# Optimization experiments

Measured on AMD Instinct MI355X. Metric: run time of the kernel, lower is better.

## Reference

```python
import jax, jax.numpy as jnp
import numpy as np

N = 1_000_000          # query points
L = 6                  # positional encoding terms
ND = 3                 # n_dims
C = 16                 # n_features
G = 96                 # feature grid resolution per axis
NODES = 128            # decoder width
IN_DIM = C + L * ND * 2  # 52
VOL_MIN, VOL_MAX = 0.0, 1.0


def setup_inputs() -> dict:
    key = jax.random.key(0)
    ks = jax.random.split(key, 8)
    x = jax.random.uniform(ks[0], (N, ND), jnp.float32, minval=-1.0, maxval=1.0)
    feature_grid = jax.random.uniform(ks[1], (C, G, G, G), jnp.float32)  # torch.rand init
    s = 0.05
    w_in = jax.random.normal(ks[2], (IN_DIM, NODES), jnp.float32) * s
    w_h0 = jax.random.normal(ks[3], (NODES, NODES), jnp.float32) * s
    w_h1 = jax.random.normal(ks[4], (NODES, NODES), jnp.float32) * s
    w_h2 = jax.random.normal(ks[5], (NODES, NODES), jnp.float32) * s
    w_out = jax.random.normal(ks[6], (NODES, 1), jnp.float32) * s
    return {"x": x, "feature_grid": feature_grid, "w_in": w_in,
            "w_h0": w_h0, "w_h1": w_h1, "w_h2": w_h2, "w_out": w_out}


def _trilinear(grid, pts):
    """grid_sample 3D, bilinear, align_corners=True. grid [C,D,H,W], pts [N,3]
    with channel order (x->W, y->H, z->D) as in torch. Returns [N, C]."""
    Cc, D, H, W = grid.shape
    fx = (pts[:, 0] + 1.0) * 0.5 * (W - 1)
    fy = (pts[:, 1] + 1.0) * 0.5 * (H - 1)
    fz = (pts[:, 2] + 1.0) * 0.5 * (D - 1)
    x0 = jnp.floor(fx); y0 = jnp.floor(fy); z0 = jnp.floor(fz)
    tx = fx - x0; ty = fy - y0; tz = fz - z0
    x0i = jnp.clip(x0.astype(jnp.int32), 0, W - 1); x1i = jnp.clip(x0i + 1, 0, W - 1)
    y0i = jnp.clip(y0.astype(jnp.int32), 0, H - 1); y1i = jnp.clip(y0i + 1, 0, H - 1)
    z0i = jnp.clip(z0.astype(jnp.int32), 0, D - 1); z1i = jnp.clip(z0i + 1, 0, D - 1)

    def g(zi, yi, xi):
        return grid[:, zi, yi, xi].T  # [N, C]

    c000 = g(z0i, y0i, x0i); c001 = g(z0i, y0i, x1i)
    c010 = g(z0i, y1i, x0i); c011 = g(z0i, y1i, x1i)
    c100 = g(z1i, y0i, x0i); c101 = g(z1i, y0i, x1i)
    c110 = g(z1i, y1i, x0i); c111 = g(z1i, y1i, x1i)
    tx = tx[:, None]; ty = ty[:, None]; tz = tz[:, None]
    c00 = c000 * (1 - tx) + c001 * tx
    c01 = c010 * (1 - tx) + c011 * tx
    c10 = c100 * (1 - tx) + c101 * tx
    c11 = c110 * (1 - tx) + c111 * tx
    c0 = c00 * (1 - ty) + c01 * ty
    c1 = c10 * (1 - ty) + c11 * ty
    return c0 * (1 - tz) + c1 * tz


def _pos_enc(pts):
    # [N, L*ND*2]: sin/cos of pi * 2^k * x for k in 0..L-1
    freqs = (jnp.pi * (2.0 ** jnp.arange(L, dtype=jnp.float32)))  # [L]
    ang = pts[:, None, :] * freqs[None, :, None]                   # [N, L, ND]
    pe = jnp.concatenate([jnp.sin(ang), jnp.cos(ang)], axis=-1)    # [N, L, 2*ND]
    return pe.reshape(pts.shape[0], -1)


def reference(x, feature_grid, w_in, w_h0, w_h1, w_h2, w_out):
    feats = _trilinear(feature_grid, x)          # [N, C]
    pe = _pos_enc(x)                             # [N, 2*L*ND]
    h = jnp.concatenate([pe, feats], axis=1)     # [N, IN_DIM]
    h = jax.nn.relu(h @ w_in)
    h = jax.nn.relu(h @ w_h0)
    h = jax.nn.relu(h @ w_h1)
    h = jax.nn.relu(h @ w_h2)
    y = h @ w_out                                # [N, 1]
    return y * (VOL_MAX - VOL_MIN) + VOL_MIN
```

## Files before the change

### kernel.cpp

```cpp
#include <hip/hip_runtime.h>
#include <stdint.h>

typedef unsigned int uint;
typedef unsigned short ushort;

#define GD   96
#define GD2  (GD*GD)
#define GSP  (GD*GD*GD)
#define NPTS 1000000
#define WIN_ELTS 8192
#define WH_ELTS  16384
#define WFRAG_OFF (GSP*16)
#define WFRAG_N  (WIN_ELTS + 3*WH_ELTS)

#define NSLAB 8
#define SLABZ 12
#define CAP   131072
#define NSLOT (NSLAB*CAP)

#define XS_BYTE   ((size_t)(WFRAG_OFF + WFRAG_N) * 2)
#define OID_BYTE  (XS_BYTE + (size_t)NSLOT * 16)
#define CUR_BYTE  (OID_BYTE + (size_t)NSLOT * 4)

#define PW   128
#define ROWB 272
#define LDS_BYTES (4*PW*ROWB)

typedef __attribute__((ext_vector_type(8))) short short8;
typedef __attribute__((ext_vector_type(4))) float f32x4;

__device__ __forceinline__ uint f2bf(float x) {
  uint u = __float_as_uint(x);
  return (u + 0x7fffu + ((u >> 16) & 1u)) >> 16;
}

__global__ void k_grid_pack(const float* __restrict__ g, ushort* __restrict__ o) {
  int sp = blockIdx.x * 256 + threadIdx.x;
  uint pk[8];
#pragma unroll
  for (int c = 0; c < 16; c += 2) {
    float a = g[(size_t)c * GSP + sp];
    float b = g[(size_t)(c + 1) * GSP + sp];
    pk[c >> 1] = f2bf(a) | (f2bf(b) << 16);
  }
  uint4* dst = (uint4*)(o + (size_t)sp * 16);
  dst[0] = make_uint4(pk[0], pk[1], pk[2], pk[3]);
  dst[1] = make_uint4(pk[4], pk[5], pk[6], pk[7]);
}

__global__ void k_w_pack(const float* __restrict__ win, const float* __restrict__ h0,
                         const float* __restrict__ h1, const float* __restrict__ h2,
                         ushort* __restrict__ o) {
  int tid = blockIdx.x * 256 + threadIdx.x;
  int lane = (tid >> 3) & 63, j = tid & 7;
  int q = lane >> 4, cc = lane & 15;
  float v;
  if (tid < WIN_ELTS) {
    int blk = tid >> 9;
    int t = blk >> 1, s = blk & 1;
    int k = s * 32 + q * 8 + j, n = t * 16 + cc;
    v = (k < 52) ? win[k * 128 + n] : 0.f;
  } else {
    int f2 = tid - WIN_ELTS;
    int l = f2 >> 14, r = f2 & 16383;
    int blk = r >> 9;
    int t = blk >> 2, s = blk & 3;
    int k = s * 32 + q * 8 + j, n = t * 16 + cc;
    const float* w = (l == 0) ? h0 : ((l == 1) ? h1 : h2);
    v = w[k * 128 + n];
  }
  o[tid] = (ushort)f2bf(v);
}

__global__ void k_prefill(const float* __restrict__ x, float4* __restrict__ xs,
                          int* __restrict__ oid, int* __restrict__ cursor) {
  int id = blockIdx.x * 256 + threadIdx.x;
  float lx = x[(NPTS - 1) * 3 + 0];
  float ly = x[(NPTS - 1) * 3 + 1];
  float lz = x[(NPTS - 1) * 3 + 2];
  xs[id] = make_float4(lx, ly, lz, 0.f);
  oid[id] = NPTS - 1;
  if (id < NSLAB) cursor[id] = id * CAP;
}

__global__ void k_scatter(const float* __restrict__ x, float4* __restrict__ xs,
                          int* __restrict__ oid, int* __restrict__ cursor) {
  __shared__ int lc[NSLAB], lb[NSLAB];
  const int tid = threadIdx.x;
  if (tid < NSLAB) lc[tid] = 0;
  __syncthreads();
  const int pbase = blockIdx.x * 4096;
  int rk[16], sl[16];
#pragma unroll
  for (int i = 0; i < 16; ++i) {
    int p = pbase + i * 256 + tid;
    int pc = min(p, NPTS - 1);
    float pz = x[pc * 3 + 2];
    int z0i = min(max((int)floorf((pz + 1.0f) * 0.5f * 95.0f), 0), 95);
    int s = z0i / SLABZ;
    sl[i] = s;
    rk[i] = (p < NPTS) ? atomicAdd(&lc[s], 1) : -1;
  }
  __syncthreads();
  if (tid < NSLAB) lb[tid] = atomicAdd(&cursor[tid], lc[tid]);
  __syncthreads();
#pragma unroll
  for (int i = 0; i < 16; ++i) {
    int p = pbase + i * 256 + tid;
    if (p < NPTS) {
      int slot = lb[sl[i]] + rk[i];
      xs[slot] = make_float4(x[p * 3 + 0], x[p * 3 + 1], x[p * 3 + 2], 0.f);
      oid[slot] = p;
    }
  }
}

#define ACC8(off, U, W) {                                  \
  fv[(off)+0] += (W) * __uint_as_float((U).x << 16);       \
  fv[(off)+1] += (W) * __uint_as_float((U).x & 0xffff0000u);\
  fv[(off)+2] += (W) * __uint_as_float((U).y << 16);       \
  fv[(off)+3] += (W) * __uint_as_float((U).y & 0xffff0000u);\
  fv[(off)+4] += (W) * __uint_as_float((U).z << 16);       \
  fv[(off)+5] += (W) * __uint_as_float((U).z & 0xffff0000u);\
  fv[(off)+6] += (W) * __uint_as_float((U).w << 16);       \
  fv[(off)+7] += (W) * __uint_as_float((U).w & 0xffff0000u);\
}

#define MFMA(A,B,C) __builtin_amdgcn_mfma_f32_16x16x32_bf16((A),(B),(C),0,0,0)

__global__ __launch_bounds__(256, 1) void k_main(
    const float4* __restrict__ xs, const int* __restrict__ oid,
    const float* __restrict__ wout,
    const ushort* __restrict__ gridb, const ushort* __restrict__ wfrag,
    float* __restrict__ out) {
  extern __shared__ char smem[];
  const int wave = threadIdx.x >> 6;
  const int lane = threadIdx.x & 63;
  const int q = lane >> 4, c = lane & 15;
  char* act = smem + wave * (PW * ROWB);
  const int b = blockIdx.x;
  const int base = (b & 7) * CAP + (b >> 3) * 512 + wave * PW;

#pragma unroll
  for (int pp = 0; pp < 2; ++pp) {
    const int p = pp * 64 + lane;
    const float4 c4 = xs[base + p];
    const float px = c4.x;
    const float py = c4.y;
    const float pz = c4.z;
    float fx = (px + 1.0f) * 0.5f * 95.0f;
    float fy = (py + 1.0f) * 0.5f * 95.0f;
    float fz = (pz + 1.0f) * 0.5f * 95.0f;
    float x0f = floorf(fx), y0f = floorf(fy), z0f = floorf(fz);
    float tx = fx - x0f, ty = fy - y0f, tz = fz - z0f;
    int x0i = min(max((int)x0f, 0), 95);
    int y0i = min(max((int)y0f, 0), 95);
    int z0i = min(max((int)z0f, 0), 95);
    int x1i = min(x0i + 1, 95);
    int y1i = min(y0i + 1, 95);
    int z1i = min(z0i + 1, 95);
    float fv[16];
#pragma unroll
    for (int k = 0; k < 16; ++k) fv[k] = 0.f;
#pragma unroll
    for (int dz = 0; dz < 2; ++dz) {
      const int zi = dz ? z1i : z0i;
      const float wz = dz ? tz : (1.f - tz);
#pragma unroll
      for (int dy = 0; dy < 2; ++dy) {
        const int yi = dy ? y1i : y0i;
        const float wzy = wz * (dy ? ty : (1.f - ty));
        const ushort* r0 = gridb + (size_t)(zi * GD2 + yi * GD + x0i) * 16;
        const ushort* r1 = gridb + (size_t)(zi * GD2 + yi * GD + x1i) * 16;
        uint4 a0 = *(const uint4*)r0;
        uint4 a1 = *(const uint4*)(r0 + 8);
        uint4 b0 = *(const uint4*)r1;
        uint4 b1 = *(const uint4*)(r1 + 8);
        const float w0 = wzy * (1.f - tx), w1 = wzy * tx;
        ACC8(0, a0, w0); ACC8(8, a1, w0);
        ACC8(0, b0, w1); ACC8(8, b1, w1);
      }
    }
    float row[64];
#pragma unroll
    for (int i = 0; i < 6; ++i) {
      const float fr = 3.14159265358979323846f * (float)(1 << i);
      row[i*6+0] = __sinf(px*fr); row[i*6+1] = __sinf(py*fr); row[i*6+2] = __sinf(pz*fr);
      row[i*6+3] = __cosf(px*fr); row[i*6+4] = __cosf(py*fr); row[i*6+5] = __cosf(pz*fr);
    }
#pragma unroll
    for (int k = 0; k < 16; ++k) row[36 + k] = fv[k];
#pragma unroll
    for (int k = 52; k < 64; ++k) row[k] = 0.f;
    char* dst = act + p * ROWB;
#pragma unroll
    for (int k = 0; k < 64; k += 8) {
      uint u0 = f2bf(row[k+0]) | (f2bf(row[k+1]) << 16);
      uint u1 = f2bf(row[k+2]) | (f2bf(row[k+3]) << 16);
      uint u2 = f2bf(row[k+4]) | (f2bf(row[k+5]) << 16);
      uint u3 = f2bf(row[k+6]) | (f2bf(row[k+7]) << 16);
      *(uint4*)(dst + k * 2) = make_uint4(u0, u1, u2, u3);
    }
  }
  asm volatile("s_waitcnt lgkmcnt(0)" ::: "memory");

  {
    short8 bw[16];
#pragma unroll
    for (int f = 0; f < 16; ++f)
      bw[f] = *(const short8*)(wfrag + f * 512 + lane * 8);
    const char* ar0 = act + c * ROWB + q * 16;
    short8 a0 = *(const short8*)(ar0);
    short8 a1 = *(const short8*)(ar0 + 64);
    for (int mt = 0; mt < 8; ++mt) {
      const short8 ca0 = a0, ca1 = a1;
      if (mt < 7) {
        const char* arn = act + ((mt + 1) * 16 + c) * ROWB + q * 16;
        a0 = *(const short8*)(arn);
        a1 = *(const short8*)(arn + 64);
      }
      f32x4 av[8];
#pragma unroll
      for (int t = 0; t < 8; ++t) av[t] = f32x4{0.f, 0.f, 0.f, 0.f};
#pragma unroll
      for (int t = 0; t < 8; ++t) {
        av[t] = MFMA(ca0, bw[t*2+0], av[t]);
        av[t] = MFMA(ca1, bw[t*2+1], av[t]);
      }
      asm volatile("s_waitcnt lgkmcnt(0)" ::: "memory");
      char* yb = act + (mt * 16 + q * 4) * ROWB + c * 2;
#pragma unroll
      for (int t = 0; t < 8; ++t)
#pragma unroll
        for (int r = 0; r < 4; ++r)
          *(ushort*)(yb + r * ROWB + t * 32) = (ushort)f2bf(fmaxf(av[t][r], 0.f));
    }
  }
  asm volatile("s_waitcnt lgkmcnt(0)" ::: "memory");

  for (int l = 0; l < 3; ++l) {
    const ushort* wl = wfrag + WIN_ELTS + l * WH_ELTS;
    short8 bw[32];
#pragma unroll
    for (int f = 0; f < 32; ++f)
      bw[f] = *(const short8*)(wl + f * 512 + lane * 8);
    if (l < 2) {
      const char* ar0 = act + c * ROWB + q * 16;
      short8 a0 = *(const short8*)(ar0);
      short8 a1 = *(const short8*)(ar0 + 64);
      short8 a2 = *(const short8*)(ar0 + 128);
      short8 a3 = *(const short8*)(ar0 + 192);
      for (int mt = 0; mt < 8; ++mt) {
        const short8 ca0 = a0, ca1 = a1, ca2 = a2, ca3 = a3;
        if (mt < 7) {
          const char* arn = act + ((mt + 1) * 16 + c) * ROWB + q * 16;
          a0 = *(const short8*)(arn);
          a1 = *(const short8*)(arn + 64);
          a2 = *(const short8*)(arn + 128);
          a3 = *(const short8*)(arn + 192);
        }
        f32x4 av[8];
#pragma unroll
        for (int t = 0; t < 8; ++t) av[t] = f32x4{0.f, 0.f, 0.f, 0.f};
#pragma unroll
        for (int t = 0; t < 8; ++t) {
          av[t] = MFMA(ca0, bw[t*4+0], av[t]);
          av[t] = MFMA(ca1, bw[t*4+1], av[t]);
          av[t] = MFMA(ca2, bw[t*4+2], av[t]);
          av[t] = MFMA(ca3, bw[t*4+3], av[t]);
        }
        asm volatile("s_waitcnt lgkmcnt(0)" ::: "memory");
        char* yb = act + (mt * 16 + q * 4) * ROWB + c * 2;
#pragma unroll
        for (int t = 0; t < 8; ++t)
#pragma unroll
          for (int r = 0; r < 4; ++r)
            *(ushort*)(yb + r * ROWB + t * 32) = (ushort)f2bf(fmaxf(av[t][r], 0.f));
      }
      asm volatile("s_waitcnt lgkmcnt(0)" ::: "memory");
    } else {
      float wo[8];
#pragma unroll
      for (int t = 0; t < 8; ++t) wo[t] = wout[t * 16 + c];
      const char* ar0 = act + c * ROWB + q * 16;
      short8 a0 = *(const short8*)(ar0);
      short8 a1 = *(const short8*)(ar0 + 64);
      short8 a2 = *(const short8*)(ar0 + 128);
      short8 a3 = *(const short8*)(ar0 + 192);
      for (int mt = 0; mt < 8; ++mt) {
        const short8 ca0 = a0, ca1 = a1, ca2 = a2, ca3 = a3;
        if (mt < 7) {
          const char* arn = act + ((mt + 1) * 16 + c) * ROWB + q * 16;
          a0 = *(const short8*)(arn);
          a1 = *(const short8*)(arn + 64);
          a2 = *(const short8*)(arn + 128);
          a3 = *(const short8*)(arn + 192);
        }
        f32x4 av[8];
#pragma unroll
        for (int t = 0; t < 8; ++t) av[t] = f32x4{0.f, 0.f, 0.f, 0.f};
#pragma unroll
        for (int t = 0; t < 8; ++t) {
          av[t] = MFMA(ca0, bw[t*4+0], av[t]);
          av[t] = MFMA(ca1, bw[t*4+1], av[t]);
          av[t] = MFMA(ca2, bw[t*4+2], av[t]);
          av[t] = MFMA(ca3, bw[t*4+3], av[t]);
        }
#pragma unroll
        for (int r = 0; r < 4; ++r) {
          float y = 0.f;
#pragma unroll
          for (int t = 0; t < 8; ++t) y += fmaxf(av[t][r], 0.f) * wo[t];
          y += __shfl_xor(y, 1, 64);
          y += __shfl_xor(y, 2, 64);
          y += __shfl_xor(y, 4, 64);
          y += __shfl_xor(y, 8, 64);
          if (c == r) {
            int slot = base + mt * 16 + q * 4 + r;
            out[oid[slot]] = y;
          }
        }
      }
    }
  }
}

extern "C" void kernel_launch(void* const* d_in, const int* in_sizes, int n_in,
                              void* d_out, int out_size, void* d_ws, size_t ws_size,
                              hipStream_t stream) {
  const float* x    = (const float*)d_in[0];
  const float* fg   = (const float*)d_in[1];
  const float* win  = (const float*)d_in[2];
  const float* wh0  = (const float*)d_in[3];
  const float* wh1  = (const float*)d_in[4];
  const float* wh2  = (const float*)d_in[5];
  const float* wout = (const float*)d_in[6];
  float* out = (float*)d_out;

  char* wsb = (char*)d_ws;
  ushort* gridb  = (ushort*)d_ws;
  ushort* wfrag  = (ushort*)d_ws + WFRAG_OFF;
  float4* xs     = (float4*)(wsb + XS_BYTE);
  int*    oid    = (int*)(wsb + OID_BYTE);
  int*    cursor = (int*)(wsb + CUR_BYTE);

  k_grid_pack<<<GSP / 256, 256, 0, stream>>>(fg, gridb);
  k_w_pack<<<(WIN_ELTS + 3 * WH_ELTS) / 256, 256, 0, stream>>>(win, wh0, wh1, wh2, wfrag);
  k_prefill<<<NSLOT / 256, 256, 0, stream>>>(x, xs, oid, cursor);
  k_scatter<<<(NPTS + 4095) / 4096, 256, 0, stream>>>(x, xs, oid, cursor);

  k_main<<<NSLAB * (CAP / 512), 256, LDS_BYTES, stream>>>(xs, oid, wout, gridb, wfrag, out);
}
```

Baseline: 411.2 us.

## Software-pipeline MLP layers with double accumulators over paired 16-row tiles

```diff
diff --git a/kernel.cpp b/kernel.cpp
--- a/kernel.cpp
+++ b/kernel.cpp
@@ -128,6 +128,59 @@
 
 #define MFMA(A,B,C) __builtin_amdgcn_mfma_f32_16x16x32_bf16((A),(B),(C),0,0,0)
 
+#define HREAD(P, A0,A1,A2,A3, B0,B1,B2,B3) {               \
+  const char* ap_ = act + ((P)*32 + c) * ROWB + q * 16;    \
+  const char* bp_ = ap_ + 16 * ROWB;                       \
+  A0 = *(const short8*)(ap_);       A1 = *(const short8*)(ap_ + 64);  \
+  A2 = *(const short8*)(ap_ + 128); A3 = *(const short8*)(ap_ + 192); \
+  B0 = *(const short8*)(bp_);       B1 = *(const short8*)(bp_ + 64);  \
+  B2 = *(const short8*)(bp_ + 128); B3 = *(const short8*)(bp_ + 192); \
+}
+
+#define HZERO2(AVA, AVB) { _Pragma("unroll")               \
+  for (int t = 0; t < 8; ++t) { AVA[t] = f32x4{0.f,0.f,0.f,0.f}; AVB[t] = f32x4{0.f,0.f,0.f,0.f}; } }
+
+#define HMFMA2(A0,A1,A2,A3, B0,B1,B2,B3, AVA, AVB) { _Pragma("unroll") \
+  for (int t = 0; t < 8; ++t) {                            \
+    AVA[t] = MFMA(A0, bw[t*4+0], AVA[t]);                  \
+    AVA[t] = MFMA(A1, bw[t*4+1], AVA[t]);                  \
+    AVA[t] = MFMA(A2, bw[t*4+2], AVA[t]);                  \
+    AVA[t] = MFMA(A3, bw[t*4+3], AVA[t]);                  \
+    AVB[t] = MFMA(B0, bw[t*4+0], AVB[t]);                  \
+    AVB[t] = MFMA(B1, bw[t*4+1], AVB[t]);                  \
+    AVB[t] = MFMA(B2, bw[t*4+2], AVB[t]);                  \
+    AVB[t] = MFMA(B3, bw[t*4+3], AVB[t]); } }
+
+#define IMFMA2(A0,A1, B0,B1, AVA, AVB) { _Pragma("unroll") \
+  for (int t = 0; t < 8; ++t) {                            \
+    AVA[t] = MFMA(A0, bwin[t*2+0], AVA[t]);                \
+    AVA[t] = MFMA(A1, bwin[t*2+1], AVA[t]);                \
+    AVB[t] = MFMA(B0, bwin[t*2+0], AVB[t]);                \
+    AVB[t] = MFMA(B1, bwin[t*2+1], AVB[t]); } }
+
+#define HEPI(P, AVA, AVB) {                                \
+  char* yA_ = act + ((P)*32 + q * 4) * ROWB + c * 2;       \
+  char* yB_ = yA_ + 16 * ROWB;                             \
+  _Pragma("unroll") for (int t = 0; t < 8; ++t)            \
+    _Pragma("unroll") for (int r = 0; r < 4; ++r) {        \
+      *(ushort*)(yA_ + r * ROWB + t * 32) = (ushort)f2bf(fmaxf(AVA[t][r], 0.f)); \
+      *(ushort*)(yB_ + r * ROWB + t * 32) = (ushort)f2bf(fmaxf(AVB[t][r], 0.f)); } }
+
+#define OEPI(P, AVA, AVB) { _Pragma("unroll")              \
+  for (int r = 0; r < 4; ++r) {                            \
+    float yA = 0.f, yB = 0.f;                              \
+    _Pragma("unroll") for (int t = 0; t < 8; ++t) {        \
+      yA += fmaxf(AVA[t][r], 0.f) * wo[t];                 \
+      yB += fmaxf(AVB[t][r], 0.f) * wo[t]; }               \
+    yA += __shfl_xor(yA, 1, 64); yA += __shfl_xor(yA, 2, 64); \
+    yA += __shfl_xor(yA, 4, 64); yA += __shfl_xor(yA, 8, 64); \
+    yB += __shfl_xor(yB, 1, 64); yB += __shfl_xor(yB, 2, 64); \
+    yB += __shfl_xor(yB, 4, 64); yB += __shfl_xor(yB, 8, 64); \
+    if (c == r) {                                          \
+      int slotA = base + (P)*32 + q * 4 + r;               \
+      out[oid[slotA]] = yA;                                \
+      out[oid[slotA + 16]] = yB; } } }
+
 __global__ __launch_bounds__(256, 1) void k_main(
     const float4* __restrict__ xs, const int* __restrict__ oid,
     const float* __restrict__ wout,
@@ -140,6 +193,14 @@
   char* act = smem + wave * (PW * ROWB);
   const int b = blockIdx.x;
   const int base = (b & 7) * CAP + (b >> 3) * 512 + wave * PW;
+
+  short8 bwin[16];
+#pragma unroll
+  for (int f = 0; f < 16; ++f)
+    bwin[f] = *(const short8*)(wfrag + f * 512 + lane * 8);
+  float wo[8];
+#pragma unroll
+  for (int t = 0; t < 8; ++t) wo[t] = wout[t * 16 + c];
 
 #pragma unroll
   for (int pp = 0; pp < 2; ++pp) {
@@ -205,36 +266,44 @@
   asm volatile("s_waitcnt lgkmcnt(0)" ::: "memory");
 
   {
-    short8 bw[16];
-#pragma unroll
-    for (int f = 0; f < 16; ++f)
-      bw[f] = *(const short8*)(wfrag + f * 512 + lane * 8);
-    const char* ar0 = act + c * ROWB + q * 16;
-    short8 a0 = *(const short8*)(ar0);
-    short8 a1 = *(const short8*)(ar0 + 64);
-    for (int mt = 0; mt < 8; ++mt) {
-      const short8 ca0 = a0, ca1 = a1;
-      if (mt < 7) {
-        const char* arn = act + ((mt + 1) * 16 + c) * ROWB + q * 16;
-        a0 = *(const short8*)(arn);
-        a1 = *(const short8*)(arn + 64);
-      }
-      f32x4 av[8];
-#pragma unroll
-      for (int t = 0; t < 8; ++t) av[t] = f32x4{0.f, 0.f, 0.f, 0.f};
-#pragma unroll
-      for (int t = 0; t < 8; ++t) {
-        av[t] = MFMA(ca0, bw[t*2+0], av[t]);
-        av[t] = MFMA(ca1, bw[t*2+1], av[t]);
-      }
-      asm volatile("s_waitcnt lgkmcnt(0)" ::: "memory");
-      char* yb = act + (mt * 16 + q * 4) * ROWB + c * 2;
-#pragma unroll
-      for (int t = 0; t < 8; ++t)
-#pragma unroll
-        for (int r = 0; r < 4; ++r)
-          *(ushort*)(yb + r * ROWB + t * 32) = (ushort)f2bf(fmaxf(av[t][r], 0.f));
-    }
+    short8 xA0, xA1, xB0, xB1, yA0, yA1, yB0, yB1;
+    f32x4 ac0A[8], ac0B[8], ac1A[8], ac1B[8];
+    {
+      const char* ap_ = act + c * ROWB + q * 16;
+      const char* bp_ = ap_ + 16 * ROWB;
+      xA0 = *(const short8*)(ap_); xA1 = *(const short8*)(ap_ + 64);
+      xB0 = *(const short8*)(bp_); xB1 = *(const short8*)(bp_ + 64);
+    }
+    HZERO2(ac0A, ac0B);
+    IMFMA2(xA0, xA1, xB0, xB1, ac0A, ac0B);
+    {
+      const char* ap_ = act + (32 + c) * ROWB + q * 16;
+      const char* bp_ = ap_ + 16 * ROWB;
+      yA0 = *(const short8*)(ap_); yA1 = *(const short8*)(ap_ + 64);
+      yB0 = *(const short8*)(bp_); yB1 = *(const short8*)(bp_ + 64);
+    }
+    HZERO2(ac1A, ac1B);
+    HEPI(0, ac0A, ac0B);
+    IMFMA2(yA0, yA1, yB0, yB1, ac1A, ac1B);
+    {
+      const char* ap_ = act + (64 + c) * ROWB + q * 16;
+      const char* bp_ = ap_ + 16 * ROWB;
+      xA0 = *(const short8*)(ap_); xA1 = *(const short8*)(ap_ + 64);
+      xB0 = *(const short8*)(bp_); xB1 = *(const short8*)(bp_ + 64);
+    }
+    HZERO2(ac0A, ac0B);
+    HEPI(1, ac1A, ac1B);
+    IMFMA2(xA0, xA1, xB0, xB1, ac0A, ac0B);
+    {
+      const char* ap_ = act + (96 + c) * ROWB + q * 16;
+      const char* bp_ = ap_ + 16 * ROWB;
+      yA0 = *(const short8*)(ap_); yA1 = *(const short8*)(ap_ + 64);
+      yB0 = *(const short8*)(bp_); yB1 = *(const short8*)(bp_ + 64);
+    }
+    HZERO2(ac1A, ac1B);
+    HEPI(2, ac0A, ac0B);
+    IMFMA2(yA0, yA1, yB0, yB1, ac1A, ac1B);
+    HEPI(3, ac1A, ac1B);
   }
   asm volatile("s_waitcnt lgkmcnt(0)" ::: "memory");
 
@@ -244,83 +313,52 @@
 #pragma unroll
     for (int f = 0; f < 32; ++f)
       bw[f] = *(const short8*)(wl + f * 512 + lane * 8);
+    short8 xA0, xA1, xA2, xA3, xB0, xB1, xB2, xB3;
+    short8 yA0, yA1, yA2, yA3, yB0, yB1, yB2, yB3;
+    f32x4 ac0A[8], ac0B[8], ac1A[8], ac1B[8];
     if (l < 2) {
-      const char* ar0 = act + c * ROWB + q * 16;
-      short8 a0 = *(const short8*)(ar0);
-      short8 a1 = *(const short8*)(ar0 + 64);
-      short8 a2 = *(const short8*)(ar0 + 128);
-      short8 a3 = *(const short8*)(ar0 + 192);
-      for (int mt = 0; mt < 8; ++mt) {
-        const short8 ca0 = a0, ca1 = a1, ca2 = a2, ca3 = a3;
-        if (mt < 7) {
-          const char* arn = act + ((mt + 1) * 16 + c) * ROWB + q * 16;
-          a0 = *(const short8*)(arn);
-          a1 = *(const short8*)(arn + 64);
-          a2 = *(const short8*)(arn + 128);
-          a3 = *(const short8*)(arn + 192);
-        }
-        f32x4 av[8];
-#pragma unroll
-        for (int t = 0; t < 8; ++t) av[t] = f32x4{0.f, 0.f, 0.f, 0.f};
-#pragma unroll
-        for (int t = 0; t < 8; ++t) {
-          av[t] = MFMA(ca0, bw[t*4+0], av[t]);
-          av[t] = MFMA(ca1, bw[t*4+1], av[t]);
-          av[t] = MFMA(ca2, bw[t*4+2], av[t]);
-          av[t] = MFMA(ca3, bw[t*4+3], av[t]);
-        }
-        asm volatile("s_waitcnt lgkmcnt(0)" ::: "memory");
-        char* yb = act + (mt * 16 + q * 4) * ROWB + c * 2;
-#pragma unroll
-        for (int t = 0; t < 8; ++t)
-#pragma unroll
-          for (int r = 0; r < 4; ++r)
-            *(ushort*)(yb + r * ROWB + t * 32) = (ushort)f2bf(fmaxf(av[t][r], 0.f));
-      }
+      HREAD(0, xA0, xA1, xA2, xA3, xB0, xB1, xB2, xB3);
+      HZERO2(ac0A, ac0B);
+      HMFMA2(xA0, xA1, xA2, xA3, xB0, xB1, xB2, xB3, ac0A, ac0B);
+
+      HREAD(1, yA0, yA1, yA2, yA3, yB0, yB1, yB2, yB3);
+      HZERO2(ac1A, ac1B);
+      HEPI(0, ac0A, ac0B);
+      HMFMA2(yA0, yA1, yA2, yA3, yB0, yB1, yB2, yB3, ac1A, ac1B);
+
+      HREAD(2, xA0, xA1, xA2, xA3, xB0, xB1, xB2, xB3);
+      HZERO2(ac0A, ac0B);
+      HEPI(1, ac1A, ac1B);
+      HMFMA2(xA0, xA1, xA2, xA3, xB0, xB1, xB2, xB3, ac0A, ac0B);
+
+      HREAD(3, yA0, yA1, yA2, yA3, yB0, yB1, yB2, yB3);
+      HZERO2(ac1A, ac1B);
+      HEPI(2, ac0A, ac0B);
+      HMFMA2(yA0, yA1, yA2, yA3, yB0, yB1, yB2, yB3, ac1A, ac1B);
+
+      HEPI(3, ac1A, ac1B);
       asm volatile("s_waitcnt lgkmcnt(0)" ::: "memory");
     } else {
-      float wo[8];
-#pragma unroll
-      for (int t = 0; t < 8; ++t) wo[t] = wout[t * 16 + c];
-      const char* ar0 = act + c * ROWB + q * 16;
-      short8 a0 = *(const short8*)(ar0);
-      short8 a1 = *(const short8*)(ar0 + 64);
-      short8 a2 = *(const short8*)(ar0 + 128);
-      short8 a3 = *(const short8*)(ar0 + 192);
-      for (int mt = 0; mt < 8; ++mt) {
-        const short8 ca0 = a0, ca1 = a1, ca2 = a2, ca3 = a3;
-        if (mt < 7) {
-          const char* arn = act + ((mt + 1) * 16 + c) * ROWB + q * 16;
-          a0 = *(const short8*)(arn);
-          a1 = *(const short8*)(arn + 64);
-          a2 = *(const short8*)(arn + 128);
-          a3 = *(const short8*)(arn + 192);
-        }
-        f32x4 av[8];
-#pragma unroll
-        for (int t = 0; t < 8; ++t) av[t] = f32x4{0.f, 0.f, 0.f, 0.f};
-#pragma unroll
-        for (int t = 0; t < 8; ++t) {
-          av[t] = MFMA(ca0, bw[t*4+0], av[t]);
-          av[t] = MFMA(ca1, bw[t*4+1], av[t]);
-          av[t] = MFMA(ca2, bw[t*4+2], av[t]);
-          av[t] = MFMA(ca3, bw[t*4+3], av[t]);
-        }
-#pragma unroll
-        for (int r = 0; r < 4; ++r) {
-          float y = 0.f;
-#pragma unroll
-          for (int t = 0; t < 8; ++t) y += fmaxf(av[t][r], 0.f) * wo[t];
-          y += __shfl_xor(y, 1, 64);
-          y += __shfl_xor(y, 2, 64);
-          y += __shfl_xor(y, 4, 64);
-          y += __shfl_xor(y, 8, 64);
-          if (c == r) {
-            int slot = base + mt * 16 + q * 4 + r;
-            out[oid[slot]] = y;
-          }
-        }
-      }
+      HREAD(0, xA0, xA1, xA2, xA3, xB0, xB1, xB2, xB3);
+      HZERO2(ac0A, ac0B);
+      HMFMA2(xA0, xA1, xA2, xA3, xB0, xB1, xB2, xB3, ac0A, ac0B);
+
+      HREAD(1, yA0, yA1, yA2, yA3, yB0, yB1, yB2, yB3);
+      HZERO2(ac1A, ac1B);
+      OEPI(0, ac0A, ac0B);
+      HMFMA2(yA0, yA1, yA2, yA3, yB0, yB1, yB2, yB3, ac1A, ac1B);
+
+      HREAD(2, xA0, xA1, xA2, xA3, xB0, xB1, xB2, xB3);
+      HZERO2(ac0A, ac0B);
+      OEPI(1, ac1A, ac1B);
+      HMFMA2(xA0, xA1, xA2, xA3, xB0, xB1, xB2, xB3, ac0A, ac0B);
+
+      HREAD(3, yA0, yA1, yA2, yA3, yB0, yB1, yB2, yB3);
+      HZERO2(ac1A, ac1B);
+      OEPI(2, ac0A, ac0B);
+      HMFMA2(yA0, yA1, yA2, yA3, yB0, yB1, yB2, yB3, ac1A, ac1B);
+
+      OEPI(3, ac1A, ac1B);
     }
   }
 }
```

After: 386.3 us. -6.1%, faster.
